# Performance work log

Measured on AMD Instinct MI355X. Metric: run time of the kernel, lower is better.

## Reference

```python
import jax, jax.numpy as jnp
import numpy as np

B, V, D, H, E = 512, 128, 256, 4, 2
Dh = D // H

def setup_inputs() -> dict:
    key = jax.random.key(0)
    k = jax.random.split(key, 8)
    x = jax.random.normal(k[0], (B, V, D), dtype=jnp.float32)
    adj = jax.random.randint(k[1], (V, V), 0, 2, dtype=jnp.int32)
    adj = adj.at[jnp.arange(V), jnp.arange(V)].set(1)  # self loops so no empty columns for real nodes
    edge_attr = jax.random.normal(k[2], (V, V, E), dtype=jnp.float32)
    mask = jax.random.bernoulli(k[3], 0.1, (B, V))  # True = padded view
    # learned params (torch Linear: y = x @ W.T)
    W = jax.random.normal(k[4], (D, D), dtype=jnp.float32) / np.sqrt(D)
    a = jax.random.normal(k[5], (2 * Dh,), dtype=jnp.float32) / np.sqrt(2 * Dh)  # attn.weight flattened
    Ew = jax.random.normal(k[6], (H, E), dtype=jnp.float32) / np.sqrt(E)  # edge_proj.weight
    return {"x": x, "adj": adj, "edge_attr": edge_attr, "mask": mask, "W": W, "a": a, "Ew": Ew}

def reference(x, adj, edge_attr, mask, W, a, Ew):
    Bv, Vv, Dv = x.shape
    Hh = Ew.shape[0]
    Dhh = Dv // Hh
    Wx = (x @ W.T).reshape(Bv, Vv, Hh, Dhh)                 # [B,V,H,Dh]
    a_src, a_dst = a[:Dhh], a[Dhh:]
    s_src = jnp.einsum('bvhd,d->bvh', Wx, a_src)             # a^T[Wh_i ; .]
    s_dst = jnp.einsum('bvhd,d->bvh', Wx, a_dst)             # a^T[. ; Wh_j]
    ef = jnp.einsum('ije,he->ijh', edge_attr, Ew)            # [V,V,H]
    e = s_src[:, :, None, :] + s_dst[:, None, :, :] + ef[None]  # [B,i,j,H]
    e = jnp.where(e >= 0, e, 0.2 * e)                        # leaky_relu(0.2)
    valid = (adj.astype(bool))[None, :, :, None] & (~mask)[:, :, None, None] & (~mask)[:, None, :, None]
    e = jnp.where(valid, e, -jnp.inf)
    # softmax over source dim i (axis=1), safe for all-masked columns (-> 0, like nan_to_num)
    m = jnp.max(e, axis=1, keepdims=True)
    m = jnp.where(jnp.isfinite(m), m, 0.0)
    p = jnp.where(valid, jnp.exp(e - m), 0.0)
    denom = jnp.sum(p, axis=1, keepdims=True)
    alpha = p / jnp.where(denom == 0, 1.0, denom)            # [B,i,j,H]
    h = jnp.einsum('bijh,bihd->bjhd', alpha, Wx).reshape(Bv, Vv, Dv)
    h = jax.nn.elu(h)
    return jnp.where(mask[:, :, None], 0.0, h)
```

## Files before the change

kernel.cpp:

```cpp
#include <hip/hip_runtime.h>
#include <hip/hip_bf16.h>
#include <cmath>

#define BB 512
#define VV 128
#define DD 256
#define HH 4
#define DHH 64

typedef unsigned short u16;
typedef __attribute__((ext_vector_type(8))) short bf16x8;
typedef __attribute__((ext_vector_type(4))) short bf16x4;
typedef __attribute__((ext_vector_type(4))) float f32x4;

__device__ __forceinline__ unsigned pk2(float a, float b) {
    __hip_bfloat162 h = __float22bfloat162_rn(make_float2(a, b));
    unsigned r;
    __builtin_memcpy(&r, &h, sizeof(r));
    return r;
}

__global__ __launch_bounds__(256) void k_ef(const float* __restrict__ ea,
                                            const float* __restrict__ Ew,
                                            const int* __restrict__ adj,
                                            float* __restrict__ efmT) {
    const int h = blockIdx.y;
    const int t = threadIdx.x;
    const int i = t & 127, jl = t >> 7;
    const float e0 = Ew[h * 2], e1 = Ew[h * 2 + 1];
    #pragma unroll
    for (int q = 0; q < 2; ++q) {
        const int j = blockIdx.x * 4 + q * 2 + jl;
        const int ij = i * VV + j;
        float v = -INFINITY;
        if (adj[ij]) v = fmaf(ea[ij * 2 + 1], e1, ea[ij * 2] * e0);
        efmT[((size_t)h * VV + j) * VV + i] = v;
    }
}

__global__ __launch_bounds__(256, 4) void k_fused(
    const float* __restrict__ x, const float* __restrict__ Wm,
    const float* __restrict__ a, const float* __restrict__ efmT,
    const int* __restrict__ mask, float* __restrict__ out) {
    __shared__ u16 ubuf[128 * 136];
    __shared__ float ssl[256], sdl[256], rden[2][128];
    __shared__ int mkl[128];

    u16* As  = ubuf;
    u16* Bs  = ubuf + 128 * 40;
    u16* WxL = ubuf;

    const int t = threadIdx.x;
    const int b = blockIdx.x, hp = blockIdx.y;
    const int w = t >> 6, L = t & 63;
    const int wr = w >> 1, wc = w & 1;
    const int lr = L & 15, lg = L >> 4;

    if (t < 128) mkl[t] = mask[b * VV + t];

    const int row = t >> 1, seg = t & 1;
    const float* xs = x  + ((size_t)b * VV + row) * DD + seg * 16;
    const float* ws = Wm + ((size_t)(hp * 128 + row)) * DD + seg * 16;
    u16* adst = As + row * 40 + seg * 16;
    u16* bdst = Bs + row * 40 + seg * 16;

    f32x4 acc[4][4];
    #pragma unroll
    for (int i = 0; i < 4; ++i)
        #pragma unroll
        for (int j = 0; j < 4; ++j) acc[i][j] = (f32x4){0.f, 0.f, 0.f, 0.f};

    float4 px[4], pw[4];
    #pragma unroll
    for (int q = 0; q < 4; ++q) {
        px[q] = *(const float4*)(xs + q * 4);
        pw[q] = *(const float4*)(ws + q * 4);
    }

    for (int ks = 0; ks < 8; ++ks) {
        unsigned va[4], vb[4], qa[4], qb[4];
        va[0] = pk2(px[0].x, px[0].y); va[1] = pk2(px[0].z, px[0].w);
        va[2] = pk2(px[1].x, px[1].y); va[3] = pk2(px[1].z, px[1].w);
        vb[0] = pk2(px[2].x, px[2].y); vb[1] = pk2(px[2].z, px[2].w);
        vb[2] = pk2(px[3].x, px[3].y); vb[3] = pk2(px[3].z, px[3].w);
        qa[0] = pk2(pw[0].x, pw[0].y); qa[1] = pk2(pw[0].z, pw[0].w);
        qa[2] = pk2(pw[1].x, pw[1].y); qa[3] = pk2(pw[1].z, pw[1].w);
        qb[0] = pk2(pw[2].x, pw[2].y); qb[1] = pk2(pw[2].z, pw[2].w);
        qb[2] = pk2(pw[3].x, pw[3].y); qb[3] = pk2(pw[3].z, pw[3].w);
        *(bf16x8*)adst       = *(bf16x8*)&va[0];
        *(bf16x8*)(adst + 8) = *(bf16x8*)&vb[0];
        *(bf16x8*)bdst       = *(bf16x8*)&qa[0];
        *(bf16x8*)(bdst + 8) = *(bf16x8*)&qb[0];
        __syncthreads();
        if (ks < 7) {
            #pragma unroll
            for (int q = 0; q < 4; ++q) {
                px[q] = *(const float4*)(xs + (ks + 1) * 32 + q * 4);
                pw[q] = *(const float4*)(ws + (ks + 1) * 32 + q * 4);
            }
        }
        bf16x8 af[4], bfr[4];
        #pragma unroll
        for (int mi = 0; mi < 4; ++mi)
            af[mi] = *(const bf16x8*)&As[(wr * 64 + mi * 16 + lr) * 40 + lg * 8];
        #pragma unroll
        for (int ni = 0; ni < 4; ++ni)
            bfr[ni] = *(const bf16x8*)&Bs[(wc * 64 + ni * 16 + lr) * 40 + lg * 8];
        #pragma unroll
        for (int mi = 0; mi < 4; ++mi)
            #pragma unroll
            for (int ni = 0; ni < 4; ++ni)
                acc[mi][ni] = __builtin_amdgcn_mfma_f32_16x16x32_bf16(
                    af[mi], bfr[ni], acc[mi][ni], 0, 0, 0);
        __syncthreads();
    }

    float as_[4], ad_[4];
    #pragma unroll
    for (int ni = 0; ni < 4; ++ni) {
        as_[ni] = a[ni * 16 + lr];
        ad_[ni] = a[64 + ni * 16 + lr];
    }
    float ps[16], pd[16];
    #pragma unroll
    for (int k = 0; k < 16; ++k) { ps[k] = 0.f; pd[k] = 0.f; }
    #pragma unroll
    for (int mi = 0; mi < 4; ++mi) {
        #pragma unroll
        for (int ni = 0; ni < 4; ++ni) {
            const int c  = wc * 64 + ni * 16 + lr;
            const int vb = wr * 64 + mi * 16 + lg * 4;
            unsigned o2[2];
            o2[0] = pk2(acc[mi][ni][0], acc[mi][ni][1]);
            o2[1] = pk2(acc[mi][ni][2], acc[mi][ni][3]);
            #pragma unroll
            for (int r = 0; r < 4; ++r) {
                float v = acc[mi][ni][r];
                ps[mi * 4 + r] = fmaf(v, as_[ni], ps[mi * 4 + r]);
                pd[mi * 4 + r] = fmaf(v, ad_[ni], pd[mi * 4 + r]);
            }
            *(uint2*)&WxL[c * 136 + vb] = *(uint2*)&o2[0];
        }
    }
    #pragma unroll
    for (int k = 0; k < 16; ++k) {
        #pragma unroll
        for (int m = 1; m < 16; m <<= 1) {
            ps[k] += __shfl_xor(ps[k], m);
            pd[k] += __shfl_xor(pd[k], m);
        }
    }
    if (lr == 0) {
        #pragma unroll
        for (int mi = 0; mi < 4; ++mi)
            #pragma unroll
            for (int r = 0; r < 4; ++r) {
                int v = wr * 64 + mi * 16 + lg * 4 + r;
                bool mk = mkl[v] != 0;
                ssl[wc * 128 + v] = mk ? -INFINITY : ps[mi * 4 + r];
                sdl[wc * 128 + v] = mk ? -INFINITY : pd[mi * 4 + r];
            }
    }
    __syncthreads();

    const int j0 = w * 32 + lr;
    for (int hl = 0; hl < 2; ++hl) {
        const int h = hp * 2 + hl;
        const float sdj0 = sdl[hl * 128 + j0];
        const float sdj1 = sdl[hl * 128 + j0 + 16];
        const float* ef0 = efmT + ((size_t)h * VV + j0) * VV;
        const float* ef1 = ef0 + 16 * VV;
        bf16x8 af2[2][4];
        float ps0 = 0.f, ps1 = 0.f;
        #pragma unroll
        for (int ks = 0; ks < 4; ++ks) {
            const int i0 = ks * 32 + lg * 8;
            float sv[8], ev0[8], ev1[8];
            *(float4*)&sv[0]  = *(const float4*)&ssl[hl * 128 + i0];
            *(float4*)&sv[4]  = *(const float4*)&ssl[hl * 128 + i0 + 4];
            *(float4*)&ev0[0] = *(const float4*)(ef0 + i0);
            *(float4*)&ev0[4] = *(const float4*)(ef0 + i0 + 4);
            *(float4*)&ev1[0] = *(const float4*)(ef1 + i0);
            *(float4*)&ev1[4] = *(const float4*)(ef1 + i0 + 4);
            float p0[8], p1[8];
            #pragma unroll
            for (int u = 0; u < 8; ++u) {
                float e0 = sv[u] + sdj0 + ev0[u];
                float e1 = sv[u] + sdj1 + ev1[u];
                e0 = fmaxf(e0, 0.2f * e0);
                e1 = fmaxf(e1, 0.2f * e1);
                p0[u] = __expf(e0); ps0 += p0[u];
                p1[u] = __expf(e1); ps1 += p1[u];
            }
            unsigned* a0 = (unsigned*)&af2[0][ks];
            unsigned* a1 = (unsigned*)&af2[1][ks];
            a0[0] = pk2(p0[0], p0[1]); a0[1] = pk2(p0[2], p0[3]);
            a0[2] = pk2(p0[4], p0[5]); a0[3] = pk2(p0[6], p0[7]);
            a1[0] = pk2(p1[0], p1[1]); a1[1] = pk2(p1[2], p1[3]);
            a1[2] = pk2(p1[4], p1[5]); a1[3] = pk2(p1[6], p1[7]);
        }
        ps0 += __shfl_xor(ps0, 16); ps0 += __shfl_xor(ps0, 32);
        ps1 += __shfl_xor(ps1, 16); ps1 += __shfl_xor(ps1, 32);
        if (lg == 0) {
            rden[hl][j0]      = ps0 > 0.f ? 1.f / ps0 : 0.f;
            rden[hl][j0 + 16] = ps1 > 0.f ? 1.f / ps1 : 0.f;
        }

        f32x4 acc2[2][4];
        #pragma unroll
        for (int mi = 0; mi < 2; ++mi)
            #pragma unroll
            for (int ni = 0; ni < 4; ++ni) acc2[mi][ni] = (f32x4){0.f, 0.f, 0.f, 0.f};
        #pragma unroll
        for (int ks = 0; ks < 4; ++ks) {
            const int kk = ks * 32 + lg * 8;
            #pragma unroll
            for (int ni = 0; ni < 4; ++ni) {
                bf16x8 bf2 = *(const bf16x8*)&WxL[(hl * 64 + ni * 16 + lr) * 136 + kk];
                acc2[0][ni] = __builtin_amdgcn_mfma_f32_16x16x32_bf16(
                    af2[0][ks], bf2, acc2[0][ni], 0, 0, 0);
                acc2[1][ni] = __builtin_amdgcn_mfma_f32_16x16x32_bf16(
                    af2[1][ks], bf2, acc2[1][ni], 0, 0, 0);
            }
        }
        __syncthreads();

        #pragma unroll
        for (int mi = 0; mi < 2; ++mi)
            #pragma unroll
            for (int ni = 0; ni < 4; ++ni) {
                const int dcol = ni * 16 + lr;
                const int jb   = w * 32 + mi * 16 + lg * 4;
                float* op = out + ((size_t)b * VV + jb) * DD + h * DHH + dcol;
                #pragma unroll
                for (int r = 0; r < 4; ++r) {
                    float v = acc2[mi][ni][r] * rden[hl][jb + r];
                    v = v > 0.f ? v : (__expf(v) - 1.0f);
                    op[(size_t)r * DD] = v;
                }
            }
    }
}

extern "C" void kernel_launch(void* const* d_in, const int* in_sizes, int n_in,
                              void* d_out, int out_size, void* d_ws, size_t ws_size,
                              hipStream_t stream) {
    const float* x    = (const float*)d_in[0];
    const int*   adj  = (const int*)d_in[1];
    const float* ea   = (const float*)d_in[2];
    const int*   mask = (const int*)d_in[3];
    const float* Wm   = (const float*)d_in[4];
    const float* a    = (const float*)d_in[5];
    const float* Ew   = (const float*)d_in[6];
    float* out = (float*)d_out;

    float* efmT = (float*)d_ws;

    k_ef<<<dim3(VV / 4, HH), 256, 0, stream>>>(ea, Ew, adj, efmT);
    k_fused<<<dim3(BB, 2), 256, 0, stream>>>(x, Wm, a, efmT, mask, out);
}
```

Measured before the change: 153.2 us.

## Transpose edge scores via shared tile, stop prefetching W, drop trailing barrier

The edge-score kernel now stages a 32x32 tile in shared memory so that both the adjacency/edge reads and the transposed writes are coalesced, where previously the writes were strided. In the fused kernel the W slice is no longer prefetched one step ahead; it is loaded at the top of each k-step, which frees registers but exposes load latency. A __syncthreads after the second MFMA loop is removed, which is safe only if shared memory is not reused before the next barrier.

```diff
diff --git a/kernel.cpp b/kernel.cpp
--- a/kernel.cpp
+++ b/kernel.cpp
@@ -10,7 +10,6 @@
 
 typedef unsigned short u16;
 typedef __attribute__((ext_vector_type(8))) short bf16x8;
-typedef __attribute__((ext_vector_type(4))) short bf16x4;
 typedef __attribute__((ext_vector_type(4))) float f32x4;
 
 __device__ __forceinline__ unsigned pk2(float a, float b) {
@@ -24,17 +23,26 @@
                                             const float* __restrict__ Ew,
                                             const int* __restrict__ adj,
                                             float* __restrict__ efmT) {
-    const int h = blockIdx.y;
+    __shared__ float tile[32][33];
+    const int jt = blockIdx.x, it = blockIdx.y, h = blockIdx.z;
     const int t = threadIdx.x;
-    const int i = t & 127, jl = t >> 7;
     const float e0 = Ew[h * 2], e1 = Ew[h * 2 + 1];
-    #pragma unroll
-    for (int q = 0; q < 2; ++q) {
-        const int j = blockIdx.x * 4 + q * 2 + jl;
+    const int jl = t & 31, il = t >> 5;
+    #pragma unroll
+    for (int p = 0; p < 4; ++p) {
+        const int i = it * 32 + p * 8 + il;
+        const int j = jt * 32 + jl;
         const int ij = i * VV + j;
         float v = -INFINITY;
         if (adj[ij]) v = fmaf(ea[ij * 2 + 1], e1, ea[ij * 2] * e0);
-        efmT[((size_t)h * VV + j) * VV + i] = v;
+        tile[p * 8 + il][jl] = v;
+    }
+    __syncthreads();
+    const int i2 = t & 31, j2 = t >> 5;
+    #pragma unroll
+    for (int p = 0; p < 4; ++p) {
+        const int j = p * 8 + j2;
+        efmT[((size_t)h * VV + jt * 32 + j) * VV + it * 32 + i2] = tile[i2][j];
     }
 }
 
@@ -70,34 +78,34 @@
         #pragma unroll
         for (int j = 0; j < 4; ++j) acc[i][j] = (f32x4){0.f, 0.f, 0.f, 0.f};
 
-    float4 px[4], pw[4];
-    #pragma unroll
-    for (int q = 0; q < 4; ++q) {
+    float4 px[4];
+    #pragma unroll
+    for (int q = 0; q < 4; ++q)
         px[q] = *(const float4*)(xs + q * 4);
-        pw[q] = *(const float4*)(ws + q * 4);
-    }
 
     for (int ks = 0; ks < 8; ++ks) {
+        float4 qw[4];
+        #pragma unroll
+        for (int q = 0; q < 4; ++q)
+            qw[q] = *(const float4*)(ws + ks * 32 + q * 4);
         unsigned va[4], vb[4], qa[4], qb[4];
         va[0] = pk2(px[0].x, px[0].y); va[1] = pk2(px[0].z, px[0].w);
         va[2] = pk2(px[1].x, px[1].y); va[3] = pk2(px[1].z, px[1].w);
         vb[0] = pk2(px[2].x, px[2].y); vb[1] = pk2(px[2].z, px[2].w);
         vb[2] = pk2(px[3].x, px[3].y); vb[3] = pk2(px[3].z, px[3].w);
-        qa[0] = pk2(pw[0].x, pw[0].y); qa[1] = pk2(pw[0].z, pw[0].w);
-        qa[2] = pk2(pw[1].x, pw[1].y); qa[3] = pk2(pw[1].z, pw[1].w);
-        qb[0] = pk2(pw[2].x, pw[2].y); qb[1] = pk2(pw[2].z, pw[2].w);
-        qb[2] = pk2(pw[3].x, pw[3].y); qb[3] = pk2(pw[3].z, pw[3].w);
         *(bf16x8*)adst       = *(bf16x8*)&va[0];
         *(bf16x8*)(adst + 8) = *(bf16x8*)&vb[0];
+        qa[0] = pk2(qw[0].x, qw[0].y); qa[1] = pk2(qw[0].z, qw[0].w);
+        qa[2] = pk2(qw[1].x, qw[1].y); qa[3] = pk2(qw[1].z, qw[1].w);
+        qb[0] = pk2(qw[2].x, qw[2].y); qb[1] = pk2(qw[2].z, qw[2].w);
+        qb[2] = pk2(qw[3].x, qw[3].y); qb[3] = pk2(qw[3].z, qw[3].w);
         *(bf16x8*)bdst       = *(bf16x8*)&qa[0];
         *(bf16x8*)(bdst + 8) = *(bf16x8*)&qb[0];
         __syncthreads();
         if (ks < 7) {
             #pragma unroll
-            for (int q = 0; q < 4; ++q) {
+            for (int q = 0; q < 4; ++q)
                 px[q] = *(const float4*)(xs + (ks + 1) * 32 + q * 4);
-                pw[q] = *(const float4*)(ws + (ks + 1) * 32 + q * 4);
-            }
         }
         bf16x8 af[4], bfr[4];
         #pragma unroll
@@ -223,7 +231,6 @@
                     af2[1][ks], bf2, acc2[1][ni], 0, 0, 0);
             }
         }
-        __syncthreads();
 
         #pragma unroll
         for (int mi = 0; mi < 2; ++mi)
@@ -256,6 +263,6 @@
 
     float* efmT = (float*)d_ws;
 
-    k_ef<<<dim3(VV / 4, HH), 256, 0, stream>>>(ea, Ew, adj, efmT);
+    k_ef<<<dim3(4, 4, HH), 256, 0, stream>>>(ea, Ew, adj, efmT);
     k_fused<<<dim3(BB, 2), 256, 0, stream>>>(x, Wm, a, efmT, mask, out);
 }
```

Measured after the change: 154.3 us. Within noise of the previous version (+0.7%).
